# Kernel tuning notes

Hardware: AMD Instinct MI355X
Metric: run time of the kernel (lower is better)

Reference implementation:

```python
import jax, jax.numpy as jnp
import numpy as np

TOP_K = 2

def setup_inputs() -> dict:
    key = jax.random.key(0)
    ks = jax.random.split(key, 6)
    B, S, H, F, E = 2, 2048, 1024, 4096, 8
    s = 0.02
    return {
        "hidden_states": jax.random.normal(ks[0], (B, S, H), dtype=jnp.float32),
        "router_w": jax.random.normal(ks[1], (H, E), dtype=jnp.float32) * s,
        "w1": jax.random.normal(ks[2], (E, H, F), dtype=jnp.float32) * s,
        "b1": jax.random.normal(ks[3], (E, F), dtype=jnp.float32) * s,
        "w2": jax.random.normal(ks[4], (E, F, H), dtype=jnp.float32) * s,
        "b2": jax.random.normal(ks[5], (E, H), dtype=jnp.float32) * s,
    }

def reference(hidden_states, router_w, w1, b1, w2, b2):
    B, S, H = hidden_states.shape
    E = w1.shape[0]
    x = hidden_states.reshape(-1, H)                      # [T, H]
    T = x.shape[0]
    # Router: sigmoid scores, top-k selection (top-1 max path is the k=1 special case)
    scores = jax.nn.sigmoid(x @ router_w)                 # [T, E]
    top_probs, top_idx = jax.lax.top_k(scores, TOP_K)     # [T, K]
    # Dense gate matrix: gate[t, e] = sum_k top_probs[t, k] * (top_idx[t, k] == e)
    gate = jnp.zeros((T, E), dtype=x.dtype).at[jnp.arange(T)[:, None], top_idx].add(top_probs)
    # Run every expert over all tokens (dense reference for the masked gather/scatter loop)
    h = jnp.einsum('th,ehf->etf', x, w1) + b1[:, None, :]  # [E, T, F]
    h = jax.nn.gelu(h, approximate=False)
    y = jnp.einsum('etf,efh->eth', h, w2) + b2[:, None, :]  # [E, T, H]
    out = jnp.einsum('te,eth->th', gate, y)                 # weighted combine
    # dropout with resid_pdrop=0.0 (inference) is identity
    return out.reshape(B, S, H)
```

## Files before the change

kernel.cpp:

```cpp
#include <hip/hip_runtime.h>
#include <math.h>

#define T_TOK 4096
#define HDIM  1024
#define FDIM  4096
#define NEXP  8
#define SLOT_CAP 9216

typedef __bf16 bf16x8 __attribute__((ext_vector_type(8)));
typedef __bf16 bf16x4 __attribute__((ext_vector_type(4)));
typedef float  f32x4  __attribute__((ext_vector_type(4)));

__device__ __forceinline__ void gload_lds16(const void* g, void* l) {
  __builtin_amdgcn_global_load_lds((const __attribute__((address_space(1))) void*)g,
                                   (__attribute__((address_space(3))) void*)l,
                                   16, 0, 0);
}

__global__ void router_k(const float* __restrict__ x, const float* __restrict__ rw,
                         __bf16* __restrict__ xb, int* __restrict__ cnt,
                         int* __restrict__ tok_e, int* __restrict__ tok_pos,
                         float* __restrict__ tok_gate) {
  const int wv   = threadIdx.x >> 6;
  const int lane = threadIdx.x & 63;
  const int t = blockIdx.x * 4 + wv;
  const float* xr = x + (size_t)t * HDIM;
  __bf16* xbr = xb + (size_t)t * HDIM;
  float acc[8];
#pragma unroll
  for (int e = 0; e < 8; ++e) acc[e] = 0.0f;
#pragma unroll
  for (int i = 0; i < 16; ++i) {
    int h = lane + (i << 6);
    float xv = xr[h];
    xbr[h] = (__bf16)xv;
    const float4* rp = (const float4*)(rw + h * 8);
    float4 r0 = rp[0], r1 = rp[1];
    acc[0] += xv * r0.x; acc[1] += xv * r0.y; acc[2] += xv * r0.z; acc[3] += xv * r0.w;
    acc[4] += xv * r1.x; acc[5] += xv * r1.y; acc[6] += xv * r1.z; acc[7] += xv * r1.w;
  }
#pragma unroll
  for (int s = 32; s >= 1; s >>= 1) {
#pragma unroll
    for (int e = 0; e < 8; ++e) acc[e] += __shfl_xor(acc[e], s, 64);
  }
  if (lane == 0) {
    float v0 = acc[0]; int b0 = 0;
#pragma unroll
    for (int e = 1; e < 8; ++e) { if (acc[e] > v0) { v0 = acc[e]; b0 = e; } }
    float v1 = -1e30f; int b1i = 0;
#pragma unroll
    for (int e = 0; e < 8; ++e) { if (e != b0 && acc[e] > v1) { v1 = acc[e]; b1i = e; } }
    float g0 = 1.0f / (1.0f + expf(-v0));
    float g1 = 1.0f / (1.0f + expf(-v1));
    int p0 = atomicAdd(&cnt[b0], 1);
    int p1 = atomicAdd(&cnt[b1i], 1);
    tok_e[t * 2] = b0;    tok_e[t * 2 + 1] = b1i;
    tok_pos[t * 2] = p0;  tok_pos[t * 2 + 1] = p1;
    tok_gate[t * 2] = g0; tok_gate[t * 2 + 1] = g1;
  }
}

__global__ void offs_k(const int* __restrict__ cnt, int* __restrict__ offs) {
  if (threadIdx.x == 0) {
    int r = 0;
    for (int e = 0; e < NEXP; ++e) { offs[e] = r; r += (cnt[e] + 127) & ~127; }
  }
}

__global__ void build_k(const int* __restrict__ tok_e, const int* __restrict__ tok_pos,
                        const float* __restrict__ tok_gate, const int* __restrict__ offs,
                        int* __restrict__ slot_tok, float* __restrict__ slot_gate) {
  int idx = blockIdx.x * blockDim.x + threadIdx.x;
  int e = tok_e[idx];
  int slot = offs[e] + tok_pos[idx];
  slot_tok[slot] = idx >> 1;
  slot_gate[slot] = tok_gate[idx];
}

__global__ void transpose_cvt(const float* __restrict__ in, __bf16* __restrict__ outp,
                              int R, int C) {
  __shared__ float tile[64][65];
  const int e = blockIdx.z;
  const int c0 = blockIdx.x * 64;
  const int r0 = blockIdx.y * 64;
  const int tr = threadIdx.x >> 4;
  const int tc4 = (threadIdx.x & 15) * 4;
  const float* ibase = in + (size_t)e * R * C;
#pragma unroll
  for (int i = 0; i < 4; ++i) {
    int r = r0 + tr + i * 16;
    float4 v = *(const float4*)(ibase + (size_t)r * C + c0 + tc4);
    tile[tr + i * 16][tc4 + 0] = v.x;
    tile[tr + i * 16][tc4 + 1] = v.y;
    tile[tr + i * 16][tc4 + 2] = v.z;
    tile[tr + i * 16][tc4 + 3] = v.w;
  }
  __syncthreads();
  __bf16* obase = outp + (size_t)e * R * C;
#pragma unroll
  for (int i = 0; i < 4; ++i) {
    int c = c0 + tr + i * 16;
    bf16x4 o;
#pragma unroll
    for (int j = 0; j < 4; ++j) o[j] = (__bf16)tile[tc4 + j][tr + i * 16];
    *(bf16x4*)(obase + (size_t)c * R + r0 + tc4) = o;
  }
}

template<bool G1>
__global__ __launch_bounds__(256) void moe_gemm(
    const __bf16* __restrict__ A, const __bf16* __restrict__ B,
    const float* __restrict__ bias,
    __bf16* __restrict__ hout, float* __restrict__ out,
    const int* __restrict__ cnt, const int* __restrict__ offs,
    const int* __restrict__ slot_tok, const float* __restrict__ slot_gate,
    int N, int K)
{
  const int e = blockIdx.z;
  const int cnt_e = cnt[e];
  const int mtile = blockIdx.y;
  if (mtile * 128 >= cnt_e) return;
  const int offs_e = offs[e];
  const int nbase = blockIdx.x * 128;

  __shared__ __bf16 As[128 * 64];
  __shared__ __bf16 Bs[128 * 64];

  const int tid = threadIdx.x;
  const int w = tid >> 6, lane = tid & 63;
  const int wy = w >> 1, wx = w & 1;
  const int lm = lane & 15, quad = lane >> 4;
  const int srow = lane >> 3;
  const int scol = lane & 7;

  const __bf16* aptr[4];
  const __bf16* bptr[4];
#pragma unroll
  for (int it = 0; it < 4; ++it) {
    int rl = w * 32 + it * 8 + srow;
    long arow;
    if constexpr (G1) {
      int gm = mtile * 128 + rl;
      int tok = (gm < cnt_e) ? slot_tok[offs_e + gm] : 0;
      arow = (long)tok;
    } else {
      arow = (long)(offs_e + mtile * 128 + rl);
    }
    aptr[it] = A + arow * (long)K + scol * 8;
    bptr[it] = B + ((long)e * N + nbase + rl) * (long)K + scol * 8;
  }

  f32x4 acc[4][4];
#pragma unroll
  for (int mt = 0; mt < 4; ++mt)
#pragma unroll
    for (int nt = 0; nt < 4; ++nt) acc[mt][nt] = (f32x4){0.f, 0.f, 0.f, 0.f};

  const int ksteps = K >> 6;
  for (int ks = 0; ks < ksteps; ++ks) {
    const int kofs = ks * 64;
#pragma unroll
    for (int it = 0; it < 4; ++it)
      gload_lds16(aptr[it] + kofs, &As[(w * 32 + it * 8) * 64]);
#pragma unroll
    for (int it = 0; it < 4; ++it)
      gload_lds16(bptr[it] + kofs, &Bs[(w * 32 + it * 8) * 64]);
    __syncthreads();

    const bf16x8* Af = reinterpret_cast<const bf16x8*>(As);
    const bf16x8* Bf = reinterpret_cast<const bf16x8*>(Bs);
#pragma unroll
    for (int kf = 0; kf < 2; ++kf) {
      bf16x8 a[4], b[4];
#pragma unroll
      for (int mt = 0; mt < 4; ++mt)
        a[mt] = Af[(wy * 64 + mt * 16 + lm) * 8 + kf * 4 + quad];
#pragma unroll
      for (int nt = 0; nt < 4; ++nt)
        b[nt] = Bf[(wx * 64 + nt * 16 + lm) * 8 + kf * 4 + quad];
#pragma unroll
      for (int mt = 0; mt < 4; ++mt)
#pragma unroll
        for (int nt = 0; nt < 4; ++nt)
          acc[mt][nt] = __builtin_amdgcn_mfma_f32_16x16x32_bf16(a[mt], b[nt], acc[mt][nt], 0, 0, 0);
    }
    __syncthreads();
  }

  if constexpr (G1) {
#pragma unroll
    for (int nt = 0; nt < 4; ++nt) {
      int n = nbase + wx * 64 + nt * 16 + lm;
      float bv = bias[e * N + n];
#pragma unroll
      for (int mt = 0; mt < 4; ++mt) {
        int mrow = wy * 64 + mt * 16 + quad * 4;
        f32x4 c = acc[mt][nt];
#pragma unroll
        for (int i = 0; i < 4; ++i) {
          int gm = mtile * 128 + mrow + i;
          if (gm < cnt_e) {
            float v = c[i] + bv;
            v = 0.5f * v * (1.0f + erff(v * 0.70710678118654752f));
            hout[(size_t)(offs_e + gm) * FDIM + n] = (__bf16)v;
          }
        }
      }
    }
  } else {
    float bv[4]; int nn[4];
#pragma unroll
    for (int nt = 0; nt < 4; ++nt) {
      nn[nt] = nbase + wx * 64 + nt * 16 + lm;
      bv[nt] = bias[e * N + nn[nt]];
    }
#pragma unroll
    for (int mt = 0; mt < 4; ++mt) {
      int mrow = wy * 64 + mt * 16 + quad * 4;
#pragma unroll
      for (int i = 0; i < 4; ++i) {
        int gm = mtile * 128 + mrow + i;
        if (gm >= cnt_e) continue;
        int slot = offs_e + gm;
        int t = slot_tok[slot];
        float g = slot_gate[slot];
        float* orow = out + (size_t)t * HDIM;
#pragma unroll
        for (int nt = 0; nt < 4; ++nt) {
          float v = acc[mt][nt][i] + bv[nt];
          atomicAdd(&orow[nn[nt]], g * v);
        }
      }
    }
  }
}

__global__ void ws_too_small_k(float* out, float v) {
  if (threadIdx.x == 0 && blockIdx.x == 0) out[0] = v;
}

extern "C" void kernel_launch(void* const* d_in, const int* in_sizes, int n_in,
                              void* d_out, int out_size, void* d_ws, size_t ws_size,
                              hipStream_t stream) {
  const float* x  = (const float*)d_in[0];
  const float* rw = (const float*)d_in[1];
  const float* w1 = (const float*)d_in[2];
  const float* b1 = (const float*)d_in[3];
  const float* w2 = (const float*)d_in[4];
  const float* b2 = (const float*)d_in[5];
  float* out = (float*)d_out;
  char* ws = (char*)d_ws;

  size_t o = 0;
  size_t o_xb = o;        o += (size_t)T_TOK * HDIM * 2;
  size_t o_w1t = o;       o += (size_t)NEXP * FDIM * HDIM * 2;
  size_t o_w2t = o;       o += (size_t)NEXP * HDIM * FDIM * 2;
  size_t o_hbuf = o;      o += (size_t)SLOT_CAP * FDIM * 2;
  size_t o_slot_tok = o;  o += (size_t)SLOT_CAP * 4;
  size_t o_slot_gate = o; o += (size_t)SLOT_CAP * 4;
  size_t o_tok_e = o;     o += (size_t)T_TOK * 2 * 4;
  size_t o_tok_pos = o;   o += (size_t)T_TOK * 2 * 4;
  size_t o_tok_gate = o;  o += (size_t)T_TOK * 2 * 4;
  size_t o_cnt = o;       o += 64;
  size_t o_offs = o;      o += 64;
  const size_t NEED = o;

  hipMemsetAsync(d_out, 0, (size_t)out_size * 4, stream);
  if (ws_size < NEED) {
    ws_too_small_k<<<1, 64, 0, stream>>>(out, (float)ws_size);
    return;
  }

  __bf16* xb   = (__bf16*)(ws + o_xb);
  __bf16* w1t  = (__bf16*)(ws + o_w1t);
  __bf16* w2t  = (__bf16*)(ws + o_w2t);
  __bf16* hbuf = (__bf16*)(ws + o_hbuf);
  int*   slot_tok  = (int*)(ws + o_slot_tok);
  float* slot_gate = (float*)(ws + o_slot_gate);
  int*   tok_e    = (int*)(ws + o_tok_e);
  int*   tok_pos  = (int*)(ws + o_tok_pos);
  float* tok_gate = (float*)(ws + o_tok_gate);
  int*   cnt  = (int*)(ws + o_cnt);
  int*   offs = (int*)(ws + o_offs);

  hipMemsetAsync(cnt, 0, 64, stream);

  transpose_cvt<<<dim3(FDIM / 64, HDIM / 64, NEXP), 256, 0, stream>>>(w1, w1t, HDIM, FDIM);
  transpose_cvt<<<dim3(HDIM / 64, FDIM / 64, NEXP), 256, 0, stream>>>(w2, w2t, FDIM, HDIM);

  router_k<<<T_TOK / 4, 256, 0, stream>>>(x, rw, xb, cnt, tok_e, tok_pos, tok_gate);
  offs_k<<<1, 64, 0, stream>>>(cnt, offs);
  build_k<<<T_TOK * 2 / 256, 256, 0, stream>>>(tok_e, tok_pos, tok_gate, offs, slot_tok, slot_gate);

  moe_gemm<true><<<dim3(FDIM / 128, 32, NEXP), 256, 0, stream>>>(
      xb, w1t, b1, hbuf, nullptr, cnt, offs, slot_tok, slot_gate, FDIM, HDIM);
  moe_gemm<false><<<dim3(HDIM / 128, 32, NEXP), 256, 0, stream>>>(
      hbuf, w2t, b2, nullptr, out, cnt, offs, slot_tok, slot_gate, HDIM, FDIM);
}
```

Before: 823.9 us.

## Compact MoE tile schedule, swizzle LDS layout, and rewrite weight transpose

The per-expert tile grid (32 m-tiles × 8 experts, mostly early-exiting) is replaced by a compact list of active (expert, m-tile) pairs built in offs_k, so the GEMM launches only as many row-blocks as needed. The LDS tiles now use an XOR swizzle on the 16-byte column chunks to avoid bank conflicts on the MFMA fragment reads. The weight transpose/convert kernel is rewritten to pack bf16 pairs in shared memory and emit 16-byte stores. Together these target wasted block launches, LDS bank conflicts and transpose store efficiency, at the cost of an extra indirection per block.

```diff
diff --git a/kernel.cpp b/kernel.cpp
--- a/kernel.cpp
+++ b/kernel.cpp
@@ -6,9 +6,9 @@
 #define FDIM  4096
 #define NEXP  8
 #define SLOT_CAP 9216
+#define MAXTILES 72
 
 typedef __bf16 bf16x8 __attribute__((ext_vector_type(8)));
-typedef __bf16 bf16x4 __attribute__((ext_vector_type(4)));
 typedef float  f32x4  __attribute__((ext_vector_type(4)));
 
 __device__ __forceinline__ void gload_lds16(const void* g, void* l) {
@@ -61,10 +61,17 @@
   }
 }
 
-__global__ void offs_k(const int* __restrict__ cnt, int* __restrict__ offs) {
+__global__ void offs_k(const int* __restrict__ cnt, int* __restrict__ offs,
+                       int* __restrict__ tile_e, int* __restrict__ tile_m) {
   if (threadIdx.x == 0) {
-    int r = 0;
-    for (int e = 0; e < NEXP; ++e) { offs[e] = r; r += (cnt[e] + 127) & ~127; }
+    int r = 0, t = 0;
+    for (int e = 0; e < NEXP; ++e) {
+      offs[e] = r;
+      int nt = (cnt[e] + 127) >> 7;
+      for (int m = 0; m < nt; ++m) { tile_e[t] = e; tile_m[t] = m; ++t; }
+      r += nt << 7;
+    }
+    for (; t < MAXTILES; ++t) { tile_e[t] = 0; tile_m[t] = 1 << 20; }
   }
 }
 
@@ -78,33 +85,37 @@
   slot_gate[slot] = tok_gate[idx];
 }
 
-__global__ void transpose_cvt(const float* __restrict__ in, __bf16* __restrict__ outp,
-                              int R, int C) {
-  __shared__ float tile[64][65];
+__global__ __launch_bounds__(256) void transpose_cvt2(const float* __restrict__ in,
+                                                      __bf16* __restrict__ outp,
+                                                      int R, int C) {
+  __shared__ unsigned int pt[32][68];
   const int e = blockIdx.z;
-  const int c0 = blockIdx.x * 64;
-  const int r0 = blockIdx.y * 64;
-  const int tr = threadIdx.x >> 4;
-  const int tc4 = (threadIdx.x & 15) * 4;
-  const float* ibase = in + (size_t)e * R * C;
-#pragma unroll
-  for (int i = 0; i < 4; ++i) {
-    int r = r0 + tr + i * 16;
-    float4 v = *(const float4*)(ibase + (size_t)r * C + c0 + tc4);
-    tile[tr + i * 16][tc4 + 0] = v.x;
-    tile[tr + i * 16][tc4 + 1] = v.y;
-    tile[tr + i * 16][tc4 + 2] = v.z;
-    tile[tr + i * 16][tc4 + 3] = v.w;
+  const int c0 = blockIdx.x * 32;
+  const int r0 = blockIdx.y * 128;
+  const int tid = threadIdx.x;
+  const float* ibase = in + (size_t)e * R * C + (size_t)r0 * C + c0;
+  const int rp = tid >> 3;
+  const int cq = (tid & 7) * 4;
+#pragma unroll
+  for (int i = 0; i < 2; ++i) {
+    int p = rp + 32 * i;
+    const float4 v0 = *(const float4*)(ibase + (size_t)(2 * p) * C + cq);
+    const float4 v1 = *(const float4*)(ibase + (size_t)(2 * p + 1) * C + cq);
+    union { __bf16 h[2]; unsigned int u; } pk;
+    pk.h[0] = (__bf16)v0.x; pk.h[1] = (__bf16)v1.x; pt[cq + 0][p] = pk.u;
+    pk.h[0] = (__bf16)v0.y; pk.h[1] = (__bf16)v1.y; pt[cq + 1][p] = pk.u;
+    pk.h[0] = (__bf16)v0.z; pk.h[1] = (__bf16)v1.z; pt[cq + 2][p] = pk.u;
+    pk.h[0] = (__bf16)v0.w; pk.h[1] = (__bf16)v1.w; pt[cq + 3][p] = pk.u;
   }
   __syncthreads();
-  __bf16* obase = outp + (size_t)e * R * C;
-#pragma unroll
-  for (int i = 0; i < 4; ++i) {
-    int c = c0 + tr + i * 16;
-    bf16x4 o;
-#pragma unroll
-    for (int j = 0; j < 4; ++j) o[j] = (__bf16)tile[tc4 + j][tr + i * 16];
-    *(bf16x4*)(obase + (size_t)c * R + r0 + tc4) = o;
+  const int rs = tid & 7;
+  const int cc = tid >> 3;
+  __bf16* obase = outp + (size_t)e * R * C + (size_t)c0 * R + r0;
+#pragma unroll
+  for (int i = 0; i < 2; ++i) {
+    int ch = rs + 8 * i;
+    uint4 v = *(const uint4*)&pt[cc][ch * 4];
+    *(uint4*)(obase + (size_t)cc * R + ch * 8) = v;
   }
 }
 
@@ -115,11 +126,12 @@
     __bf16* __restrict__ hout, float* __restrict__ out,
     const int* __restrict__ cnt, const int* __restrict__ offs,
     const int* __restrict__ slot_tok, const float* __restrict__ slot_gate,
+    const int* __restrict__ tile_e, const int* __restrict__ tile_m,
     int N, int K)
 {
-  const int e = blockIdx.z;
+  const int e = tile_e[blockIdx.y];
+  const int mtile = tile_m[blockIdx.y];
   const int cnt_e = cnt[e];
-  const int mtile = blockIdx.y;
   if (mtile * 128 >= cnt_e) return;
   const int offs_e = offs[e];
   const int nbase = blockIdx.x * 128;
@@ -131,6 +143,7 @@
   const int w = tid >> 6, lane = tid & 63;
   const int wy = w >> 1, wx = w & 1;
   const int lm = lane & 15, quad = lane >> 4;
+  const int lm7 = lane & 7;
   const int srow = lane >> 3;
   const int scol = lane & 7;
 
@@ -147,8 +160,9 @@
     } else {
       arow = (long)(offs_e + mtile * 128 + rl);
     }
-    aptr[it] = A + arow * (long)K + scol * 8;
-    bptr[it] = B + ((long)e * N + nbase + rl) * (long)K + scol * 8;
+    const int swcol = (scol ^ srow) << 3;
+    aptr[it] = A + arow * (long)K + swcol;
+    bptr[it] = B + ((long)e * N + nbase + rl) * (long)K + swcol;
   }
 
   f32x4 acc[4][4];
@@ -175,10 +189,10 @@
       bf16x8 a[4], b[4];
 #pragma unroll
       for (int mt = 0; mt < 4; ++mt)
-        a[mt] = Af[(wy * 64 + mt * 16 + lm) * 8 + kf * 4 + quad];
+        a[mt] = Af[(wy * 64 + mt * 16 + lm) * 8 + (((kf << 2) + quad) ^ lm7)];
 #pragma unroll
       for (int nt = 0; nt < 4; ++nt)
-        b[nt] = Bf[(wx * 64 + nt * 16 + lm) * 8 + kf * 4 + quad];
+        b[nt] = Bf[(wx * 64 + nt * 16 + lm) * 8 + (((kf << 2) + quad) ^ lm7)];
 #pragma unroll
       for (int mt = 0; mt < 4; ++mt)
 #pragma unroll
@@ -264,6 +278,7 @@
   size_t o_tok_gate = o;  o += (size_t)T_TOK * 2 * 4;
   size_t o_cnt = o;       o += 64;
   size_t o_offs = o;      o += 64;
+  size_t o_tile = o;      o += MAXTILES * 2 * 4;
   const size_t NEED = o;
 
   hipMemsetAsync(d_out, 0, (size_t)out_size * 4, stream);
@@ -283,18 +298,20 @@
   float* tok_gate = (float*)(ws + o_tok_gate);
   int*   cnt  = (int*)(ws + o_cnt);
   int*   offs = (int*)(ws + o_offs);
+  int*   tile_e = (int*)(ws + o_tile);
+  int*   tile_m = tile_e + MAXTILES;
 
   hipMemsetAsync(cnt, 0, 64, stream);
 
-  transpose_cvt<<<dim3(FDIM / 64, HDIM / 64, NEXP), 256, 0, stream>>>(w1, w1t, HDIM, FDIM);
-  transpose_cvt<<<dim3(HDIM / 64, FDIM / 64, NEXP), 256, 0, stream>>>(w2, w2t, FDIM, HDIM);
+  transpose_cvt2<<<dim3(FDIM / 32, HDIM / 128, NEXP), 256, 0, stream>>>(w1, w1t, HDIM, FDIM);
+  transpose_cvt2<<<dim3(HDIM / 32, FDIM / 128, NEXP), 256, 0, stream>>>(w2, w2t, FDIM, HDIM);
 
   router_k<<<T_TOK / 4, 256, 0, stream>>>(x, rw, xb, cnt, tok_e, tok_pos, tok_gate);
-  offs_k<<<1, 64, 0, stream>>>(cnt, offs);
+  offs_k<<<1, 64, 0, stream>>>(cnt, offs, tile_e, tile_m);
   build_k<<<T_TOK * 2 / 256, 256, 0, stream>>>(tok_e, tok_pos, tok_gate, offs, slot_tok, slot_gate);
 
-  moe_gemm<true><<<dim3(FDIM / 128, 32, NEXP), 256, 0, stream>>>(
-      xb, w1t, b1, hbuf, nullptr, cnt, offs, slot_tok, slot_gate, FDIM, HDIM);
-  moe_gemm<false><<<dim3(HDIM / 128, 32, NEXP), 256, 0, stream>>>(
-      hbuf, w2t, b2, nullptr, out, cnt, offs, slot_tok, slot_gate, HDIM, FDIM);
-}
+  moe_gemm<true><<<dim3(FDIM / 128, MAXTILES), 256, 0, stream>>>(
+      xb, w1t, b1, hbuf, nullptr, cnt, offs, slot_tok, slot_gate, tile_e, tile_m, FDIM, HDIM);
+  moe_gemm<false><<<dim3(HDIM / 128, MAXTILES), 256, 0, stream>>>(
+      hbuf, w2t, b2, nullptr, out, cnt, offs, slot_tok, slot_gate, tile_e, tile_m, HDIM, FDIM);
+}
```

After: 690.9 us. -16.1%, faster.
